# Optimization experiments

Hardware: AMD Instinct MI355X
Metric: run time of the kernel (lower is better)

The kernel has to match this reference:

```python
import jax, jax.numpy as jnp
import numpy as np

E = 327680      # number of edges
D_NODE = 128    # n_node_feats
D_EDGE = 128    # n_edge_feats_in
D_GLOB = 128    # n_global_feats
LATENT = 128    # latent_size
D_OUT = 128     # n_edge_feats_out
D_IN = D_EDGE + 2 * D_NODE + D_GLOB  # 512, MLP input width


def setup_inputs() -> dict:
    key = jax.random.key(0)
    ks = jax.random.split(key, 12)
    inv = lambda n: 1.0 / np.sqrt(n)
    return {
        "receiver": jax.random.normal(ks[0], (E, D_NODE), dtype=jnp.float32),
        "sender": jax.random.normal(ks[1], (E, D_NODE), dtype=jnp.float32),
        "edge_attr": jax.random.normal(ks[2], (E, D_EDGE), dtype=jnp.float32),
        "global_attr": jax.random.normal(ks[3], (1, D_GLOB), dtype=jnp.float32),
        "W1": jax.random.normal(ks[4], (D_IN, LATENT), dtype=jnp.float32) * inv(D_IN),
        "b1": jnp.zeros((LATENT,), dtype=jnp.float32),
        "W2": jax.random.normal(ks[5], (LATENT, LATENT), dtype=jnp.float32) * inv(LATENT),
        "b2": jnp.zeros((LATENT,), dtype=jnp.float32),
        "W3": jax.random.normal(ks[6], (LATENT, LATENT), dtype=jnp.float32) * inv(LATENT),
        "b3": jnp.zeros((LATENT,), dtype=jnp.float32),
        "W4": jax.random.normal(ks[7], (LATENT, D_OUT), dtype=jnp.float32) * inv(LATENT),
        "b4": jnp.zeros((D_OUT,), dtype=jnp.float32),
    }


def reference(receiver, sender, edge_attr, global_attr,
              W1, b1, W2, b2, W3, b3, W4, b4):
    e = edge_attr.shape[0]
    # pad_to_size(global_attr, E, mode='repeat'): tile rows to match edge count
    g = jnp.tile(global_attr, (e // global_attr.shape[0], 1))  # [E, D_GLOB]
    x = jnp.concatenate([receiver, sender, edge_attr, g], axis=1)  # [E, D_IN]
    h = jax.nn.relu(x @ W1 + b1)
    h = jax.nn.relu(h @ W2 + b2)
    h = jax.nn.relu(h @ W3 + b3)
    return h @ W4 + b4  # [E, D_OUT], no final activation
```

## Files before the change

kernel.cpp:

```cpp
#include <hip/hip_runtime.h>

#define E_EDGES 327680
#define D 128
#define BM 128
#define NW 4

typedef __bf16 bf16x8 __attribute__((ext_vector_type(8)));
typedef float  f32x4  __attribute__((ext_vector_type(4)));

#define L1_OFF 0
#define L2_OFF 131072
#define L3_OFF 163840
#define L4_OFF 196608
#define WS_BYTES 229376

__device__ __forceinline__ unsigned short f2bf(float f) {
  unsigned int u = __builtin_bit_cast(unsigned int, f);
  u += 0x7fffu + ((u >> 16) & 1u);
  return (unsigned short)(u >> 16);
}

__global__ __launch_bounds__(256) void prep_weights(
    const float* __restrict__ W1, const float* __restrict__ W2,
    const float* __restrict__ W3, const float* __restrict__ W4,
    unsigned short* __restrict__ ws)
{
  int tid = blockIdx.x * 256 + threadIdx.x;
  if (tid >= 224 * 64) return;
  int lane = tid & 63;
  int frag = tid >> 6;
  const float* W; int base_us; int lf;
  if (frag < 128)      { W = W1; base_us = L1_OFF / 2; lf = frag; }
  else if (frag < 160) { W = W2; base_us = L2_OFF / 2; lf = frag - 128; }
  else if (frag < 192) { W = W3; base_us = L3_OFF / 2; lf = frag - 160; }
  else                 { W = W4; base_us = L4_OFF / 2; lf = frag - 192; }
  int kb = lf >> 3, nt = lf & 7;
  int k0 = kb * 32 + (lane >> 4) * 8;
  int n  = nt * 16 + (lane & 15);
  unsigned int pk[4];
#pragma unroll
  for (int j = 0; j < 4; ++j) {
    unsigned int lo = f2bf(W[(size_t)(k0 + 2 * j    ) * D + n]);
    unsigned int hi = f2bf(W[(size_t)(k0 + 2 * j + 1) * D + n]);
    pk[j] = lo | (hi << 16);
  }
  *(uint4*)(ws + base_us + ((size_t)lf * 64 + lane) * 8) =
      make_uint4(pk[0], pk[1], pk[2], pk[3]);
}

__global__ __launch_bounds__(256) void edge_mlp(
    const float* __restrict__ recv, const float* __restrict__ send,
    const float* __restrict__ edge, const float* __restrict__ glob,
    const float* __restrict__ b1, const float* __restrict__ b2,
    const float* __restrict__ b3, const float* __restrict__ b4,
    const unsigned short* __restrict__ ws,
    float* __restrict__ out)
{
  __shared__ __attribute__((aligned(16))) char smem[NW * 8192];
  const int lane = threadIdx.x & 63;
  const int wid  = threadIdx.x >> 6;
  char* wbuf = smem + wid * 8192;
  const int row0 = blockIdx.x * BM + wid * 32;
  const int arow = lane & 15;
  const int kgrp = lane >> 4;

  f32x4 acc[2][8];
#pragma unroll
  for (int m = 0; m < 2; ++m)
#pragma unroll
    for (int n = 0; n < 8; ++n) acc[m][n] = (f32x4)0.0f;

#pragma unroll
  for (int c = 0; c < 4; ++c) {
    const float* src = (c == 0) ? recv : (c == 1) ? send : (c == 2) ? edge : glob;
#pragma unroll
    for (int i = 0; i < 16; ++i) {
      int flat = i * 64 + lane;
      int r  = flat >> 5;
      int c4 = flat & 31;
      float4 v;
      if (c == 3) v = ((const float4*)glob)[c4];
      else        v = ((const float4*)(src + (size_t)(row0 + r) * D))[c4];
      unsigned int lo = (unsigned int)f2bf(v.x) | ((unsigned int)f2bf(v.y) << 16);
      unsigned int hi = (unsigned int)f2bf(v.z) | ((unsigned int)f2bf(v.w) << 16);
      int colB = c4 * 8;
      int addr = r * 256 + (((colB & ~15) ^ ((r & 7) << 4)) | (colB & 8));
      *(uint2*)(wbuf + addr) = make_uint2(lo, hi);
    }
#pragma unroll
    for (int kk = 0; kk < 4; ++kk) {
      int kblock = c * 4 + kk;
      const unsigned short* wp = ws + L1_OFF / 2 + ((size_t)(kblock * 8) * 64 + lane) * 8;
      bf16x8 bfr[8];
#pragma unroll
      for (int n = 0; n < 8; ++n) bfr[n] = *(const bf16x8*)(wp + (size_t)n * 512);
      bf16x8 afr[2];
#pragma unroll
      for (int m = 0; m < 2; ++m) {
        int rl = m * 16 + arow;
        int kB = kk * 64 + kgrp * 16;
        afr[m] = *(const bf16x8*)(wbuf + rl * 256 + (kB ^ ((rl & 7) << 4)));
      }
#pragma unroll
      for (int m = 0; m < 2; ++m)
#pragma unroll
        for (int n = 0; n < 8; ++n)
          acc[m][n] = __builtin_amdgcn_mfma_f32_16x16x32_bf16(afr[m], bfr[n], acc[m][n], 0, 0, 0);
    }
  }

  auto store_h = [&](const float* __restrict__ bias) {
#pragma unroll
    for (int n = 0; n < 8; ++n) {
      float bn = bias[n * 16 + arow];
#pragma unroll
      for (int m = 0; m < 2; ++m) {
#pragma unroll
        for (int r = 0; r < 4; ++r) {
          float v = fmaxf(acc[m][n][r] + bn, 0.0f);
          int rw   = m * 16 + kgrp * 4 + r;
          int colB = (n * 16 + arow) * 2;
          int addr = rw * 256 + (((colB & ~15) ^ ((rw & 7) << 4)) | (colB & 15));
          *(unsigned short*)(wbuf + addr) = f2bf(v);
        }
        acc[m][n] = (f32x4)0.0f;
      }
    }
  };

  auto do_layer = [&](int ws_us_off) {
#pragma unroll
    for (int kk = 0; kk < 4; ++kk) {
      const unsigned short* wp = ws + ws_us_off + ((size_t)(kk * 8) * 64 + lane) * 8;
      bf16x8 bfr[8];
#pragma unroll
      for (int n = 0; n < 8; ++n) bfr[n] = *(const bf16x8*)(wp + (size_t)n * 512);
      bf16x8 afr[2];
#pragma unroll
      for (int m = 0; m < 2; ++m) {
        int rl = m * 16 + arow;
        int kB = kk * 64 + kgrp * 16;
        afr[m] = *(const bf16x8*)(wbuf + rl * 256 + (kB ^ ((rl & 7) << 4)));
      }
#pragma unroll
      for (int m = 0; m < 2; ++m)
#pragma unroll
        for (int n = 0; n < 8; ++n)
          acc[m][n] = __builtin_amdgcn_mfma_f32_16x16x32_bf16(afr[m], bfr[n], acc[m][n], 0, 0, 0);
    }
  };

  store_h(b1);
  do_layer(L2_OFF / 2);
  store_h(b2);
  do_layer(L3_OFF / 2);
  store_h(b3);
  do_layer(L4_OFF / 2);

#pragma unroll
  for (int n = 0; n < 8; ++n) {
    float bn = b4[n * 16 + arow];
#pragma unroll
    for (int m = 0; m < 2; ++m)
#pragma unroll
      for (int r = 0; r < 4; ++r) {
        int rw = m * 16 + kgrp * 4 + r;
        out[(size_t)(row0 + rw) * D + n * 16 + arow] = acc[m][n][r] + bn;
      }
  }
}

extern "C" void kernel_launch(void* const* d_in, const int* in_sizes, int n_in,
                              void* d_out, int out_size, void* d_ws, size_t ws_size,
                              hipStream_t stream)
{
  const float* recv = (const float*)d_in[0];
  const float* send = (const float*)d_in[1];
  const float* edge = (const float*)d_in[2];
  const float* glob = (const float*)d_in[3];
  const float* W1 = (const float*)d_in[4];
  const float* b1 = (const float*)d_in[5];
  const float* W2 = (const float*)d_in[6];
  const float* b2 = (const float*)d_in[7];
  const float* W3 = (const float*)d_in[8];
  const float* b3 = (const float*)d_in[9];
  const float* W4 = (const float*)d_in[10];
  const float* b4 = (const float*)d_in[11];
  unsigned short* ws = (unsigned short*)d_ws;

  prep_weights<<<56, 256, 0, stream>>>(W1, W2, W3, W4, ws);
  edge_mlp<<<E_EDGES / BM, 256, 0, stream>>>(recv, send, edge, glob,
                                             b1, b2, b3, b4, ws, (float*)d_out);
}
```

Before: 186.2 us.

## Fold global features into layer-1 bias and load A fragments directly from global

The constant global-feature block of the first matmul is precomputed once as glob·W1[384:512]+b1 in an extra prep block, which cuts the layer-1 K dimension from 512 to 384. Layer-1 A fragments are now read directly from global memory in MFMA layout and converted with the packed v_cvt_pk_bf16_f32 instruction, skipping the LDS staging round trip. The hidden-layer stores use the same packed conversion, and launch bounds request 4 blocks per CU. The direct loads are less coalesced (32-byte pieces per lane) and the tighter launch bounds may force register spills.

```diff
diff --git a/kernel.cpp b/kernel.cpp
--- a/kernel.cpp
+++ b/kernel.cpp
@@ -12,7 +12,7 @@
 #define L2_OFF 131072
 #define L3_OFF 163840
 #define L4_OFF 196608
-#define WS_BYTES 229376
+#define B1P_US 49152
 
 __device__ __forceinline__ unsigned short f2bf(float f) {
   unsigned int u = __builtin_bit_cast(unsigned int, f);
@@ -20,15 +20,41 @@
   return (unsigned short)(u >> 16);
 }
 
+__device__ __forceinline__ unsigned int cvtpk(float lo, float hi) {
+  unsigned int r;
+  asm("v_cvt_pk_bf16_f32 %0, %1, %2" : "=v"(r) : "v"(lo), "v"(hi));
+  return r;
+}
+
+__device__ __forceinline__ bf16x8 cvt8(float4 a, float4 b) {
+  union { unsigned int u[4]; bf16x8 v; } r;
+  r.u[0] = cvtpk(a.x, a.y);
+  r.u[1] = cvtpk(a.z, a.w);
+  r.u[2] = cvtpk(b.x, b.y);
+  r.u[3] = cvtpk(b.z, b.w);
+  return r.v;
+}
+
 __global__ __launch_bounds__(256) void prep_weights(
     const float* __restrict__ W1, const float* __restrict__ W2,
     const float* __restrict__ W3, const float* __restrict__ W4,
+    const float* __restrict__ b1, const float* __restrict__ glob,
     unsigned short* __restrict__ ws)
 {
+  if (blockIdx.x == 56) {
+    int n = threadIdx.x;
+    if (n < D) {
+      float s = b1[n];
+      for (int j = 0; j < D; ++j) s += glob[j] * W1[(size_t)(384 + j) * D + n];
+      ((float*)(ws + B1P_US))[n] = s;
+    }
+    return;
+  }
   int tid = blockIdx.x * 256 + threadIdx.x;
   if (tid >= 224 * 64) return;
   int lane = tid & 63;
   int frag = tid >> 6;
+  if (frag >= 96 && frag < 128) return;
   const float* W; int base_us; int lf;
   if (frag < 128)      { W = W1; base_us = L1_OFF / 2; lf = frag; }
   else if (frag < 160) { W = W2; base_us = L2_OFF / 2; lf = frag - 128; }
@@ -48,11 +74,11 @@
       make_uint4(pk[0], pk[1], pk[2], pk[3]);
 }
 
-__global__ __launch_bounds__(256) void edge_mlp(
+__global__ __launch_bounds__(256, 4) void edge_mlp(
     const float* __restrict__ recv, const float* __restrict__ send,
-    const float* __restrict__ edge, const float* __restrict__ glob,
-    const float* __restrict__ b1, const float* __restrict__ b2,
-    const float* __restrict__ b3, const float* __restrict__ b4,
+    const float* __restrict__ edge,
+    const float* __restrict__ b2, const float* __restrict__ b3,
+    const float* __restrict__ b4,
     const unsigned short* __restrict__ ws,
     float* __restrict__ out)
 {
@@ -71,26 +97,61 @@
     for (int n = 0; n < 8; ++n) acc[m][n] = (f32x4)0.0f;
 
 #pragma unroll
-  for (int c = 0; c < 4; ++c) {
-    const float* src = (c == 0) ? recv : (c == 1) ? send : (c == 2) ? edge : glob;
-#pragma unroll
-    for (int i = 0; i < 16; ++i) {
-      int flat = i * 64 + lane;
-      int r  = flat >> 5;
-      int c4 = flat & 31;
-      float4 v;
-      if (c == 3) v = ((const float4*)glob)[c4];
-      else        v = ((const float4*)(src + (size_t)(row0 + r) * D))[c4];
-      unsigned int lo = (unsigned int)f2bf(v.x) | ((unsigned int)f2bf(v.y) << 16);
-      unsigned int hi = (unsigned int)f2bf(v.z) | ((unsigned int)f2bf(v.w) << 16);
-      int colB = c4 * 8;
-      int addr = r * 256 + (((colB & ~15) ^ ((r & 7) << 4)) | (colB & 8));
-      *(uint2*)(wbuf + addr) = make_uint2(lo, hi);
-    }
+  for (int c = 0; c < 3; ++c) {
+    const float* src = (c == 0) ? recv : (c == 1) ? send : edge;
+    const float* p0 = src + (size_t)(row0 + arow) * D + kgrp * 8;
+    const float* p1 = p0 + (size_t)16 * D;
 #pragma unroll
     for (int kk = 0; kk < 4; ++kk) {
-      int kblock = c * 4 + kk;
-      const unsigned short* wp = ws + L1_OFF / 2 + ((size_t)(kblock * 8) * 64 + lane) * 8;
+      const unsigned short* wp =
+          ws + L1_OFF / 2 + ((size_t)((c * 4 + kk) * 8) * 64 + lane) * 8;
+      bf16x8 bfr[8];
+#pragma unroll
+      for (int n = 0; n < 8; ++n) bfr[n] = *(const bf16x8*)(wp + (size_t)n * 512);
+      bf16x8 afr[2];
+#pragma unroll
+      for (int m = 0; m < 2; ++m) {
+        const float* p = (m ? p1 : p0) + kk * 32;
+        float4 v0 = *(const float4*)p;
+        float4 v1 = *(const float4*)(p + 4);
+        afr[m] = cvt8(v0, v1);
+      }
+#pragma unroll
+      for (int m = 0; m < 2; ++m)
+#pragma unroll
+        for (int n = 0; n < 8; ++n)
+          acc[m][n] = __builtin_amdgcn_mfma_f32_16x16x32_bf16(afr[m], bfr[n], acc[m][n], 0, 0, 0);
+    }
+  }
+
+  auto store_h = [&](const float* __restrict__ bias) {
+#pragma unroll
+    for (int n = 0; n < 8; ++n) {
+      float bn = bias[n * 16 + arow];
+      int colB = (n * 16 + arow) * 2;
+#pragma unroll
+      for (int m = 0; m < 2; ++m) {
+#pragma unroll
+        for (int rp = 0; rp < 4; rp += 2) {
+          float x0 = fmaxf(acc[m][n][rp]     + bn, 0.0f);
+          float x1 = fmaxf(acc[m][n][rp + 1] + bn, 0.0f);
+          unsigned int u = cvtpk(x0, x1);
+          int rw0 = m * 16 + kgrp * 4 + rp;
+          int rw1 = rw0 + 1;
+          int a0 = rw0 * 256 + (((colB & ~15) ^ ((rw0 & 7) << 4)) | (colB & 15));
+          int a1 = rw1 * 256 + (((colB & ~15) ^ ((rw1 & 7) << 4)) | (colB & 15));
+          *(unsigned short*)(wbuf + a0) = (unsigned short)u;
+          *(unsigned short*)(wbuf + a1) = (unsigned short)(u >> 16);
+        }
+        acc[m][n] = (f32x4)0.0f;
+      }
+    }
+  };
+
+  auto do_layer = [&](int ws_us_off) {
+#pragma unroll
+    for (int kk = 0; kk < 4; ++kk) {
+      const unsigned short* wp = ws + ws_us_off + ((size_t)(kk * 8) * 64 + lane) * 8;
       bf16x8 bfr[8];
 #pragma unroll
       for (int n = 0; n < 8; ++n) bfr[n] = *(const bf16x8*)(wp + (size_t)n * 512);
@@ -107,50 +168,10 @@
         for (int n = 0; n < 8; ++n)
           acc[m][n] = __builtin_amdgcn_mfma_f32_16x16x32_bf16(afr[m], bfr[n], acc[m][n], 0, 0, 0);
     }
-  }
-
-  auto store_h = [&](const float* __restrict__ bias) {
-#pragma unroll
-    for (int n = 0; n < 8; ++n) {
-      float bn = bias[n * 16 + arow];
-#pragma unroll
-      for (int m = 0; m < 2; ++m) {
-#pragma unroll
-        for (int r = 0; r < 4; ++r) {
-          float v = fmaxf(acc[m][n][r] + bn, 0.0f);
-          int rw   = m * 16 + kgrp * 4 + r;
-          int colB = (n * 16 + arow) * 2;
-          int addr = rw * 256 + (((colB & ~15) ^ ((rw & 7) << 4)) | (colB & 15));
-          *(unsigned short*)(wbuf + addr) = f2bf(v);
-        }
-        acc[m][n] = (f32x4)0.0f;
-      }
-    }
   };
 
-  auto do_layer = [&](int ws_us_off) {
-#pragma unroll
-    for (int kk = 0; kk < 4; ++kk) {
-      const unsigned short* wp = ws + ws_us_off + ((size_t)(kk * 8) * 64 + lane) * 8;
-      bf16x8 bfr[8];
-#pragma unroll
-      for (int n = 0; n < 8; ++n) bfr[n] = *(const bf16x8*)(wp + (size_t)n * 512);
-      bf16x8 afr[2];
-#pragma unroll
-      for (int m = 0; m < 2; ++m) {
-        int rl = m * 16 + arow;
-        int kB = kk * 64 + kgrp * 16;
-        afr[m] = *(const bf16x8*)(wbuf + rl * 256 + (kB ^ ((rl & 7) << 4)));
-      }
-#pragma unroll
-      for (int m = 0; m < 2; ++m)
-#pragma unroll
-        for (int n = 0; n < 8; ++n)
-          acc[m][n] = __builtin_amdgcn_mfma_f32_16x16x32_bf16(afr[m], bfr[n], acc[m][n], 0, 0, 0);
-    }
-  };
-
-  store_h(b1);
+  const float* b1p = (const float*)(ws + B1P_US);
+  store_h(b1p);
   do_layer(L2_OFF / 2);
   store_h(b2);
   do_layer(L3_OFF / 2);
@@ -188,7 +209,7 @@
   const float* b4 = (const float*)d_in[11];
   unsigned short* ws = (unsigned short*)d_ws;
 
-  prep_weights<<<56, 256, 0, stream>>>(W1, W2, W3, W4, ws);
-  edge_mlp<<<E_EDGES / BM, 256, 0, stream>>>(recv, send, edge, glob,
-                                             b1, b2, b3, b4, ws, (float*)d_out);
-}
+  prep_weights<<<57, 256, 0, stream>>>(W1, W2, W3, W4, b1, glob, ws);
+  edge_mlp<<<E_EDGES / BM, 256, 0, stream>>>(recv, send, edge,
+                                             b2, b3, b4, ws, (float*)d_out);
+}
```

Result: slower. 313.1 us (+68.2%).

## Fold global features into bias and keep activations in registers via transposed MFMA

Applied to the files above, without the earlier changes.

Precomputes the global-attribute contribution to layer 1 (glob·W1 slice + b1) in the prep kernel, which removes a quarter of the layer-1 K dimension. Switches to 32x32x16 MFMAs in a transposed formulation (weights as A, activations as B), so each layer's output is converted to bf16 and repacked in registers with permlane32 swaps instead of going through LDS. Input rows are loaded directly from global memory into MFMA operands and stores become vectorized. Relies on gfx950-specific instructions and a specific permuted bias layout.

```diff
diff --git a/kernel.cpp b/kernel.cpp
--- a/kernel.cpp
+++ b/kernel.cpp
@@ -2,17 +2,16 @@
 
 #define E_EDGES 327680
 #define D 128
-#define BM 128
-#define NW 4
 
 typedef __bf16 bf16x8 __attribute__((ext_vector_type(8)));
 typedef float  f32x4  __attribute__((ext_vector_type(4)));
-
-#define L1_OFF 0
-#define L2_OFF 131072
-#define L3_OFF 163840
-#define L4_OFF 196608
-#define WS_BYTES 229376
+typedef float  f32x16 __attribute__((ext_vector_type(16)));
+
+#define L1F 0
+#define L2F 98304
+#define L3F 131072
+#define L4F 163840
+#define BIASPF 196608
 
 __device__ __forceinline__ unsigned short f2bf(float f) {
   unsigned int u = __builtin_bit_cast(unsigned int, f);
@@ -20,153 +19,174 @@
   return (unsigned short)(u >> 16);
 }
 
+__device__ __forceinline__ unsigned int cvtpk(float lo, float hi) {
+  unsigned int r;
+  asm("v_cvt_pk_bf16_f32 %0, %1, %2" : "=v"(r) : "v"(lo), "v"(hi));
+  return r;
+}
+
+__device__ __forceinline__ void swap32(unsigned int& a, unsigned int& b) {
+  asm("v_permlane32_swap_b32 %0, %1" : "+v"(a), "+v"(b));
+}
+
+__device__ __forceinline__ bf16x8 cvt8(f32x4 a, f32x4 b) {
+  union { unsigned int u[4]; bf16x8 v; } r;
+  r.u[0] = cvtpk(a[0], a[1]);
+  r.u[1] = cvtpk(a[2], a[3]);
+  r.u[2] = cvtpk(b[0], b[1]);
+  r.u[3] = cvtpk(b[2], b[3]);
+  return r.v;
+}
+
+__device__ __forceinline__ int bias_slot(int n) {
+  int t = n >> 5, rem = n & 31;
+  int r = rem & 3, hi = (rem >> 2) & 1, q = rem >> 3;
+  return t * 32 + hi * 16 + (r + 4 * q);
+}
+
 __global__ __launch_bounds__(256) void prep_weights(
     const float* __restrict__ W1, const float* __restrict__ W2,
     const float* __restrict__ W3, const float* __restrict__ W4,
-    unsigned short* __restrict__ ws)
+    const float* __restrict__ b1, const float* __restrict__ b2,
+    const float* __restrict__ b3, const float* __restrict__ b4,
+    const float* __restrict__ glob, char* __restrict__ ws)
 {
-  int tid = blockIdx.x * 256 + threadIdx.x;
-  if (tid >= 224 * 64) return;
+  float* biasP = (float*)(ws + BIASPF);
+  if (blockIdx.x == 48) {
+    int i = threadIdx.x;
+    if (i < 128) {
+      float s = b1[i];
+      for (int j = 0; j < 128; ++j) s += glob[j] * W1[(size_t)(384 + j) * D + i];
+      biasP[0 * 128 + bias_slot(i)] = s;
+    } else {
+      int n = i - 128;
+      biasP[1 * 128 + bias_slot(n)] = b2[n];
+      biasP[2 * 128 + bias_slot(n)] = b3[n];
+      biasP[3 * 128 + bias_slot(n)] = b4[n];
+    }
+    return;
+  }
+  int tid  = blockIdx.x * 256 + threadIdx.x;
   int lane = tid & 63;
-  int frag = tid >> 6;
-  const float* W; int base_us; int lf;
-  if (frag < 128)      { W = W1; base_us = L1_OFF / 2; lf = frag; }
-  else if (frag < 160) { W = W2; base_us = L2_OFF / 2; lf = frag - 128; }
-  else if (frag < 192) { W = W3; base_us = L3_OFF / 2; lf = frag - 160; }
-  else                 { W = W4; base_us = L4_OFF / 2; lf = frag - 192; }
-  int kb = lf >> 3, nt = lf & 7;
-  int k0 = kb * 32 + (lane >> 4) * 8;
-  int n  = nt * 16 + (lane & 15);
+  int f    = tid >> 6;
+  const float* W; int base; int lf;
+  if (f < 96)       { W = W1; base = L1F; lf = f; }
+  else if (f < 128) { W = W2; base = L2F; lf = f - 96; }
+  else if (f < 160) { W = W3; base = L3F; lf = f - 128; }
+  else              { W = W4; base = L4F; lf = f - 160; }
+  int s = lf >> 2, t = lf & 3;
+  int k0 = s * 16 + (lane >> 5) * 8;
+  int n  = t * 32 + (lane & 31);
   unsigned int pk[4];
 #pragma unroll
-  for (int j = 0; j < 4; ++j) {
-    unsigned int lo = f2bf(W[(size_t)(k0 + 2 * j    ) * D + n]);
-    unsigned int hi = f2bf(W[(size_t)(k0 + 2 * j + 1) * D + n]);
-    pk[j] = lo | (hi << 16);
-  }
-  *(uint4*)(ws + base_us + ((size_t)lf * 64 + lane) * 8) =
+  for (int p = 0; p < 4; ++p) {
+    unsigned int lo = f2bf(W[(size_t)(k0 + 2 * p    ) * D + n]);
+    unsigned int hi = f2bf(W[(size_t)(k0 + 2 * p + 1) * D + n]);
+    pk[p] = lo | (hi << 16);
+  }
+  *(uint4*)(ws + base + (size_t)(lf * 64 + lane) * 16) =
       make_uint4(pk[0], pk[1], pk[2], pk[3]);
 }
 
 __global__ __launch_bounds__(256) void edge_mlp(
     const float* __restrict__ recv, const float* __restrict__ send,
-    const float* __restrict__ edge, const float* __restrict__ glob,
-    const float* __restrict__ b1, const float* __restrict__ b2,
-    const float* __restrict__ b3, const float* __restrict__ b4,
-    const unsigned short* __restrict__ ws,
+    const float* __restrict__ edge, const char* __restrict__ ws,
     float* __restrict__ out)
 {
-  __shared__ __attribute__((aligned(16))) char smem[NW * 8192];
   const int lane = threadIdx.x & 63;
   const int wid  = threadIdx.x >> 6;
-  char* wbuf = smem + wid * 8192;
-  const int row0 = blockIdx.x * BM + wid * 32;
-  const int arow = lane & 15;
-  const int kgrp = lane >> 4;
-
-  f32x4 acc[2][8];
-#pragma unroll
-  for (int m = 0; m < 2; ++m)
-#pragma unroll
-    for (int n = 0; n < 8; ++n) acc[m][n] = (f32x4)0.0f;
-
-#pragma unroll
-  for (int c = 0; c < 4; ++c) {
-    const float* src = (c == 0) ? recv : (c == 1) ? send : (c == 2) ? edge : glob;
-#pragma unroll
-    for (int i = 0; i < 16; ++i) {
-      int flat = i * 64 + lane;
-      int r  = flat >> 5;
-      int c4 = flat & 31;
-      float4 v;
-      if (c == 3) v = ((const float4*)glob)[c4];
-      else        v = ((const float4*)(src + (size_t)(row0 + r) * D))[c4];
-      unsigned int lo = (unsigned int)f2bf(v.x) | ((unsigned int)f2bf(v.y) << 16);
-      unsigned int hi = (unsigned int)f2bf(v.z) | ((unsigned int)f2bf(v.w) << 16);
-      int colB = c4 * 8;
-      int addr = r * 256 + (((colB & ~15) ^ ((r & 7) << 4)) | (colB & 8));
-      *(uint2*)(wbuf + addr) = make_uint2(lo, hi);
-    }
-#pragma unroll
-    for (int kk = 0; kk < 4; ++kk) {
-      int kblock = c * 4 + kk;
-      const unsigned short* wp = ws + L1_OFF / 2 + ((size_t)(kblock * 8) * 64 + lane) * 8;
-      bf16x8 bfr[8];
-#pragma unroll
-      for (int n = 0; n < 8; ++n) bfr[n] = *(const bf16x8*)(wp + (size_t)n * 512);
-      bf16x8 afr[2];
-#pragma unroll
-      for (int m = 0; m < 2; ++m) {
-        int rl = m * 16 + arow;
-        int kB = kk * 64 + kgrp * 16;
-        afr[m] = *(const bf16x8*)(wbuf + rl * 256 + (kB ^ ((rl & 7) << 4)));
-      }
-#pragma unroll
-      for (int m = 0; m < 2; ++m)
-#pragma unroll
-        for (int n = 0; n < 8; ++n)
-          acc[m][n] = __builtin_amdgcn_mfma_f32_16x16x32_bf16(afr[m], bfr[n], acc[m][n], 0, 0, 0);
-    }
-  }
-
-  auto store_h = [&](const float* __restrict__ bias) {
-#pragma unroll
-    for (int n = 0; n < 8; ++n) {
-      float bn = bias[n * 16 + arow];
-#pragma unroll
-      for (int m = 0; m < 2; ++m) {
+  const int m    = lane & 31;
+  const int hi   = lane >> 5;
+  const int row0 = blockIdx.x * 128 + wid * 32;
+  const float* biasF = (const float*)(ws + BIASPF);
+
+  f32x16 acc[4];
+#pragma unroll
+  for (int t = 0; t < 4; ++t) acc[t] = (f32x16)0.0f;
+
+  bf16x8 bn[8];
+
+  auto epilogue = [&](int layerOff, bool relu) {
+#pragma unroll
+    for (int t = 0; t < 4; ++t) {
+      const float* bp = biasF + layerOff + t * 32 + hi * 16;
+      f32x16 v = acc[t];
+#pragma unroll
+      for (int q = 0; q < 4; ++q) {
+        f32x4 bq = *(const f32x4*)(bp + q * 4);
 #pragma unroll
         for (int r = 0; r < 4; ++r) {
-          float v = fmaxf(acc[m][n][r] + bn, 0.0f);
-          int rw   = m * 16 + kgrp * 4 + r;
-          int colB = (n * 16 + arow) * 2;
-          int addr = rw * 256 + (((colB & ~15) ^ ((rw & 7) << 4)) | (colB & 15));
-          *(unsigned short*)(wbuf + addr) = f2bf(v);
+          float x = v[q * 4 + r] + bq[r];
+          v[q * 4 + r] = relu ? fmaxf(x, 0.0f) : x;
         }
-        acc[m][n] = (f32x4)0.0f;
-      }
+      }
+      {
+        unsigned int u0 = cvtpk(v[0], v[1]), u1 = cvtpk(v[2], v[3]);
+        unsigned int w0 = cvtpk(v[4], v[5]), w1 = cvtpk(v[6], v[7]);
+        swap32(u0, w0); swap32(u1, w1);
+        union { unsigned int u[4]; bf16x8 b; } pk;
+        pk.u[0] = u0; pk.u[1] = u1; pk.u[2] = w0; pk.u[3] = w1;
+        bn[2 * t] = pk.b;
+      }
+      {
+        unsigned int u0 = cvtpk(v[8], v[9]),  u1 = cvtpk(v[10], v[11]);
+        unsigned int w0 = cvtpk(v[12], v[13]), w1 = cvtpk(v[14], v[15]);
+        swap32(u0, w0); swap32(u1, w1);
+        union { unsigned int u[4]; bf16x8 b; } pk;
+        pk.u[0] = u0; pk.u[1] = u1; pk.u[2] = w0; pk.u[3] = w1;
+        bn[2 * t + 1] = pk.b;
+      }
+      acc[t] = (f32x16)0.0f;
     }
   };
 
-  auto do_layer = [&](int ws_us_off) {
-#pragma unroll
-    for (int kk = 0; kk < 4; ++kk) {
-      const unsigned short* wp = ws + ws_us_off + ((size_t)(kk * 8) * 64 + lane) * 8;
-      bf16x8 bfr[8];
-#pragma unroll
-      for (int n = 0; n < 8; ++n) bfr[n] = *(const bf16x8*)(wp + (size_t)n * 512);
-      bf16x8 afr[2];
-#pragma unroll
-      for (int m = 0; m < 2; ++m) {
-        int rl = m * 16 + arow;
-        int kB = kk * 64 + kgrp * 16;
-        afr[m] = *(const bf16x8*)(wbuf + rl * 256 + (kB ^ ((rl & 7) << 4)));
-      }
-#pragma unroll
-      for (int m = 0; m < 2; ++m)
-#pragma unroll
-        for (int n = 0; n < 8; ++n)
-          acc[m][n] = __builtin_amdgcn_mfma_f32_16x16x32_bf16(afr[m], bfr[n], acc[m][n], 0, 0, 0);
+  const float* rp0 = recv + (size_t)(row0 + m) * D + hi * 8;
+  const float* rp1 = send + (size_t)(row0 + m) * D + hi * 8;
+  const float* rp2 = edge + (size_t)(row0 + m) * D + hi * 8;
+#pragma unroll
+  for (int s = 0; s < 24; ++s) {
+    const float* p = (s < 8 ? rp0 : s < 16 ? rp1 : rp2) + (s & 7) * 16;
+    f32x4 v0 = *(const f32x4*)p;
+    f32x4 v1 = *(const f32x4*)(p + 4);
+    bf16x8 b = cvt8(v0, v1);
+#pragma unroll
+    for (int t = 0; t < 4; ++t) {
+      bf16x8 a = *(const bf16x8*)(ws + L1F + (size_t)((s * 4 + t) * 64 + lane) * 16);
+      acc[t] = __builtin_amdgcn_mfma_f32_32x32x16_bf16(a, b, acc[t], 0, 0, 0);
+    }
+  }
+  epilogue(0, true);
+
+  auto do_layer = [&](int fragOff) {
+#pragma unroll
+    for (int s = 0; s < 8; ++s) {
+      bf16x8 b = bn[s];
+#pragma unroll
+      for (int t = 0; t < 4; ++t) {
+        bf16x8 a = *(const bf16x8*)(ws + fragOff + (size_t)((s * 4 + t) * 64 + lane) * 16);
+        acc[t] = __builtin_amdgcn_mfma_f32_32x32x16_bf16(a, b, acc[t], 0, 0, 0);
+      }
     }
   };
 
-  store_h(b1);
-  do_layer(L2_OFF / 2);
-  store_h(b2);
-  do_layer(L3_OFF / 2);
-  store_h(b3);
-  do_layer(L4_OFF / 2);
-
-#pragma unroll
-  for (int n = 0; n < 8; ++n) {
-    float bn = b4[n * 16 + arow];
-#pragma unroll
-    for (int m = 0; m < 2; ++m)
-#pragma unroll
-      for (int r = 0; r < 4; ++r) {
-        int rw = m * 16 + kgrp * 4 + r;
-        out[(size_t)(row0 + rw) * D + n * 16 + arow] = acc[m][n][r] + bn;
-      }
+  do_layer(L2F);
+  epilogue(128, true);
+  do_layer(L3F);
+  epilogue(256, true);
+  do_layer(L4F);
+
+#pragma unroll
+  for (int t = 0; t < 4; ++t) {
+    const float* bp = biasF + 3 * 128 + t * 32 + hi * 16;
+    float* po = out + (size_t)(row0 + m) * D + t * 32 + hi * 4;
+#pragma unroll
+    for (int q = 0; q < 4; ++q) {
+      f32x4 bq = *(const f32x4*)(bp + q * 4);
+      f32x4 sv;
+#pragma unroll
+      for (int r = 0; r < 4; ++r) sv[r] = acc[t][q * 4 + r] + bq[r];
+      *(f32x4*)(po + q * 8) = sv;
+    }
   }
 }
 
@@ -186,9 +206,8 @@
   const float* b3 = (const float*)d_in[9];
   const float* W4 = (const float*)d_in[10];
   const float* b4 = (const float*)d_in[11];
-  unsigned short* ws = (unsigned short*)d_ws;
-
-  prep_weights<<<56, 256, 0, stream>>>(W1, W2, W3, W4, ws);
-  edge_mlp<<<E_EDGES / BM, 256, 0, stream>>>(recv, send, edge, glob,
-                                             b1, b2, b3, b4, ws, (float*)d_out);
-}
+  char* ws = (char*)d_ws;
+
+  prep_weights<<<49, 256, 0, stream>>>(W1, W2, W3, W4, b1, b2, b3, b4, glob, ws);
+  edge_mlp<<<E_EDGES / 128, 256, 0, stream>>>(recv, send, edge, ws, (float*)d_out);
+}
```

New measurement: 313.3 us. 68.2% more time.
